# Optimization experiments

Hardware: AMD Instinct MI355X
Metric: run time of the kernel (lower is better)

Reference implementation:

```python
import jax, jax.numpy as jnp
import numpy as np

S, B, D, H, DFF = 1024, 4, 1024, 16, 4096
HD = D // H
EPS = 1e-5


def setup_inputs() -> dict:
    key = jax.random.key(0)
    ks = jax.random.split(key, 16)

    def w(k, shape):
        return jax.random.normal(k, shape, jnp.float32) * 0.02

    inp = {
        "input": jax.random.normal(ks[0], (S, B, D), jnp.float32),  # [seq, batch, d_model]
        "enc": jax.random.normal(ks[1], (S, B, D), jnp.float32),
    }
    i = 2
    for pfx in ("sa", "ca"):
        for name in ("wq", "wk", "wv", "wo"):
            inp[f"{pfx}_{name}"] = w(ks[i], (D, D)); i += 1
            inp[f"{pfx}_b{name[1]}"] = jnp.zeros((D,), jnp.float32)
    inp["w1"] = w(ks[i], (DFF, D)); i += 1
    inp["b1"] = jnp.zeros((DFF,), jnp.float32)
    inp["w2"] = w(ks[i], (D, DFF)); i += 1
    inp["b2"] = jnp.zeros((D,), jnp.float32)
    for n in (1, 2, 3):
        inp[f"ln{n}_g"] = jnp.ones((D,), jnp.float32)
        inp[f"ln{n}_b"] = jnp.zeros((D,), jnp.float32)
    return inp


def _layernorm(x, g, b):
    m = x.mean(-1, keepdims=True)
    v = x.var(-1, keepdims=True)
    return (x - m) * jax.lax.rsqrt(v + EPS) * g + b


def _mha(query, key, value, wq, bq, wk, bk, wv, bv, wo, bo):
    # query/key/value: [seq, batch, d_model] (seq-first layout)
    def proj(x, w, b):
        y = x @ w.T + b
        s, bsz, _ = y.shape
        return y.reshape(s, bsz, H, HD)  # [s, b, h, hd]

    q = proj(query, wq, bq)
    k = proj(key, wk, bk)
    v = proj(value, wv, bv)
    scores = jnp.einsum("sbhd,tbhd->bhst", q, k) / (HD ** 0.5)  # [b, h, s_q, s_k]
    p = jax.nn.softmax(scores, axis=-1)
    o = jnp.einsum("bhst,tbhd->sbhd", p, v)  # [s_q, b, h, hd]
    o = o.reshape(o.shape[0], o.shape[1], D)  # heads concatenated along features
    return o @ wo.T + bo  # [s_q, b, d_model]


def reference(input, enc,
              sa_wq, sa_bq, sa_wk, sa_bk, sa_wv, sa_bv, sa_wo, sa_bo,
              ca_wq, ca_bq, ca_wk, ca_bk, ca_wv, ca_bv, ca_wo, ca_bo,
              w1, b1, w2, b2,
              ln1_g, ln1_b, ln2_g, ln2_b, ln3_g, ln3_b):
    # self-attention: attn_in_1(input, input, input) -> q=k=v=input
    out1 = _mha(input, input, input, sa_wq, sa_bq, sa_wk, sa_bk, sa_wv, sa_bv, sa_wo, sa_bo)
    out = _layernorm(input + out1, ln1_g, ln1_b)
    # cross-attention: attn_in_2(out, enc, enc) binds key=out, query=enc, value=enc
    out2 = _mha(enc, out, enc, ca_wq, ca_bq, ca_wk, ca_bk, ca_wv, ca_bv, ca_wo, ca_bo)
    out = _layernorm(out + out2, ln2_g, ln2_b)
    # FFN (dropout is identity at p=0 / eval)
    out3 = jax.nn.relu(out @ w1.T + b1) @ w2.T + b2
    return _layernorm(out + out3, ln3_g, ln3_b)
```

## Files before the change

kernel.cpp:

```cpp
#include <hip/hip_runtime.h>
#include <hip/hip_bf16.h>
#include <cstdint>
#include <cstddef>


typedef __bf16 bf16;
typedef __attribute__((ext_vector_type(8))) __bf16 bf16x8;
typedef __attribute__((ext_vector_type(4))) __bf16 bf16x4;
typedef __attribute__((ext_vector_type(4))) float f32x4;

#define SEQ   1024
#define BATCH 4
#define DMOD  1024
#define NHEAD 16
#define HDIM  64
#define NTOK  (SEQ*BATCH)
#define DFF   4096

#define GLD(gp, lp) __builtin_amdgcn_global_load_lds( \
    (__attribute__((address_space(1))) void*)(gp),    \
    (__attribute__((address_space(3))) void*)(lp), 16, 0, 0)

struct CastSeg { const float* src; bf16* dst; int n4; };
struct CastArgs { CastSeg seg[12]; };

__global__ __launch_bounds__(256) void cast_multi(CastArgs a) {
  CastSeg s = a.seg[blockIdx.y];
  int i = blockIdx.x * 256 + threadIdx.x;
  if (i < s.n4) {
    float4 v = ((const float4*)s.src)[i];
    bf16x4 o; o[0] = (bf16)v.x; o[1] = (bf16)v.y; o[2] = (bf16)v.z; o[3] = (bf16)v.w;
    ((bf16x4*)s.dst)[i] = o;
  }
}

__global__ __launch_bounds__(256) void gemm_nt(
    const bf16* __restrict__ A, const bf16* __restrict__ W,
    const float* __restrict__ b0, const float* __restrict__ b1,
    const float* __restrict__ b2, const float* __restrict__ b3,
    void* __restrict__ C, int M, int N, int K, int flags, int kc)
{
  __shared__ bf16 As[4096];
  __shared__ bf16 Bs[4096];
  const int tid  = threadIdx.x;
  const int wave = tid >> 6, lane = tid & 63;
  const int quad = lane >> 4, l16 = lane & 15;
  const int m0 = blockIdx.y * 128, n0 = blockIdx.x * 128;
  const int wm = (wave >> 1) * 64, wn = (wave & 1) * 64;

  f32x4 acc[4][4] = {};

  const int srow = tid >> 2;
  const int scol = ((tid & 3) ^ ((srow >> 1) & 3)) * 8;
  const int kbeg = blockIdx.z * kc;
  const bf16* Ap = A + (size_t)(m0 + srow) * K + scol + kbeg;
  const bf16* Wp = W + (size_t)(n0 + srow) * K + scol + kbeg;
  const size_t rstep = (size_t)64 * K;
  bf16* AsW = As + wave * 512;
  bf16* BsW = Bs + wave * 512;

  const int swz = (l16 >> 1) & 3;
  const int aq = (quad ^ swz) * 8;

  for (int k0 = 0; k0 < kc; k0 += 32) {
    __syncthreads();
    GLD(Ap + k0,         AsW);
    GLD(Ap + rstep + k0, AsW + 2048);
    GLD(Wp + k0,         BsW);
    GLD(Wp + rstep + k0, BsW + 2048);
    __syncthreads();
    bf16x8 af[4], bfr[4];
#pragma unroll
    for (int i = 0; i < 4; ++i)
      af[i] = *(const bf16x8*)(As + (wm + i * 16 + l16) * 32 + aq);
#pragma unroll
    for (int i = 0; i < 4; ++i)
      bfr[i] = *(const bf16x8*)(Bs + (wn + i * 16 + l16) * 32 + aq);
#pragma unroll
    for (int mi = 0; mi < 4; ++mi)
#pragma unroll
      for (int ni = 0; ni < 4; ++ni)
        acc[mi][ni] = __builtin_amdgcn_mfma_f32_16x16x32_bf16(af[mi], bfr[ni], acc[mi][ni], 0, 0, 0);
  }

  if (gridDim.z > 1) {
    float* Cp = (float*)C + (size_t)blockIdx.z * M * N;
#pragma unroll
    for (int mi = 0; mi < 4; ++mi) {
      const int gr = m0 + wm + mi * 16 + quad * 4;
#pragma unroll
      for (int ni = 0; ni < 4; ++ni) {
        const int gc = n0 + wn + ni * 16 + l16;
#pragma unroll
        for (int r = 0; r < 4; ++r)
          Cp[(size_t)(gr + r) * N + gc] = acc[mi][ni][r];
      }
    }
    return;
  }

  const float* bp[4] = {b0, b1, b2, b3};
  const bool obf = flags & 1, orelu = flags & 2, oscale = flags & 4;
#pragma unroll
  for (int mi = 0; mi < 4; ++mi) {
    const int gr = m0 + wm + mi * 16 + quad * 4;
#pragma unroll
    for (int ni = 0; ni < 4; ++ni) {
      const int gc = n0 + wn + ni * 16 + l16;
      const float bi = bp[gc >> 10][gc & 1023];
      const float sc = (oscale && gc < 1024) ? 0.125f : 1.0f;
#pragma unroll
      for (int r = 0; r < 4; ++r) {
        float v = (acc[mi][ni][r] + bi) * sc;
        if (orelu) v = fmaxf(v, 0.0f);
        const size_t idx = (size_t)(gr + r) * N + gc;
        if (obf) ((bf16*)C)[idx] = (bf16)v;
        else     ((float*)C)[idx] = v;
      }
    }
  }
}

__global__ __launch_bounds__(256) void vtrans(
    const bf16* __restrict__ V, int ldv, bf16* __restrict__ VT)
{
  const int tid = threadIdx.x, w = tid >> 6, lane = tid & 63;
  const int b = blockIdx.y >> 4;
  const int co = (blockIdx.y & 15) * HDIM;
  const int s0 = blockIdx.x * 64;
  const int hd0 = blockIdx.z * 32 + w * 8;
  bf16x8 v = *(const bf16x8*)(V + ((size_t)(s0 + lane) * BATCH + b) * ldv + co + hd0);
  const size_t obase = ((size_t)blockIdx.y * HDIM + hd0) * SEQ + s0 + lane;
#pragma unroll
  for (int j = 0; j < 8; ++j)
    VT[obase + (size_t)j * SEQ] = v[j];
}

__global__ __launch_bounds__(256) void attn_kernel(
    const bf16* __restrict__ Q, int ldq,
    const bf16* __restrict__ K, int ldk,
    const bf16* __restrict__ VT,
    bf16* __restrict__ O)
{
  __shared__ bf16 Kt[64 * 64];
  __shared__ bf16 Vt[64 * 64];

  const int tid = threadIdx.x, w = tid >> 6, lane = tid & 63;
  const int quad = lane >> 4, l16 = lane & 15;
  const int bh = blockIdx.y, b = bh >> 4;
  const int co = (bh & 15) * HDIM;
  const int sq0 = blockIdx.x * 128 + w * 32;

  bf16x8 qf[2][2];
#pragma unroll
  for (int u = 0; u < 2; ++u) {
    const bf16* qp = Q + ((size_t)(sq0 + u * 16 + l16) * BATCH + b) * ldq + co + quad * 8;
    qf[u][0] = *(const bf16x8*)qp;
    qf[u][1] = *(const bf16x8*)(qp + 32);
  }

  f32x4 oacc[2][4] = {};
  float lsum[2] = {0.f, 0.f};

  const int srow = lane >> 3;
  const int glog = (lane & 7) ^ srow;
  const int sw = l16 & 7;

  for (int t0 = 0; t0 < SEQ; t0 += 64) {
    __syncthreads();
#pragma unroll
    for (int j = 0; j < 2; ++j) {
      const int slot = j * 32 + w * 8 + srow;
      const int m = slot & 15, half = (slot >> 4) & 1, chunk = slot >> 5;
      const int t = chunk * 32 + 8 * (m >> 2) + 4 * half + (m & 3);
      GLD(K + ((size_t)(t0 + t) * BATCH + b) * ldk + co + glog * 8,
          Kt + (j * 32 + w * 8) * 64);
      const int hd = j * 32 + w * 8 + srow;
      GLD(VT + ((size_t)bh * HDIM + hd) * SEQ + t0 + glog * 8,
          Vt + (j * 32 + w * 8) * 64);
    }
    __syncthreads();

#pragma unroll
    for (int c = 0; c < 2; ++c) {
      const bf16* k0 = Kt + (c * 32 + l16) * 64;
      const bf16* k1 = Kt + (c * 32 + 16 + l16) * 64;
      const int g0 = (quad ^ sw) * 8;
      const int g1 = ((4 + quad) ^ sw) * 8;
      bf16x8 ka00 = *(const bf16x8*)(k0 + g0);
      bf16x8 ka01 = *(const bf16x8*)(k0 + g1);
      bf16x8 ka10 = *(const bf16x8*)(k1 + g0);
      bf16x8 ka11 = *(const bf16x8*)(k1 + g1);
      bf16x8 vf[4];
#pragma unroll
      for (int nt = 0; nt < 4; ++nt)
        vf[nt] = *(const bf16x8*)(Vt + (nt * 16 + l16) * 64 + (((c * 4 + quad) ^ sw) * 8));
#pragma unroll
      for (int u = 0; u < 2; ++u) {
        f32x4 c0 = {}, c1 = {};
        c0 = __builtin_amdgcn_mfma_f32_16x16x32_bf16(ka00, qf[u][0], c0, 0, 0, 0);
        c0 = __builtin_amdgcn_mfma_f32_16x16x32_bf16(ka01, qf[u][1], c0, 0, 0, 0);
        c1 = __builtin_amdgcn_mfma_f32_16x16x32_bf16(ka10, qf[u][0], c1, 0, 0, 0);
        c1 = __builtin_amdgcn_mfma_f32_16x16x32_bf16(ka11, qf[u][1], c1, 0, 0, 0);
        bf16x8 pf; float ls = 0.f;
#pragma unroll
        for (int r = 0; r < 4; ++r) {
          float p0 = __expf(c0[r]);
          float p1 = __expf(c1[r]);
          ls += p0 + p1;
          pf[r] = (bf16)p0;
          pf[4 + r] = (bf16)p1;
        }
        lsum[u] += ls;
#pragma unroll
        for (int nt = 0; nt < 4; ++nt)
          oacc[u][nt] = __builtin_amdgcn_mfma_f32_16x16x32_bf16(pf, vf[nt], oacc[u][nt], 0, 0, 0);
      }
    }
  }

#pragma unroll
  for (int u = 0; u < 2; ++u) {
    float s = lsum[u];
    s += __shfl_xor(s, 16, 64);
    s += __shfl_xor(s, 32, 64);
#pragma unroll
    for (int r = 0; r < 4; ++r) {
      const float inv = 1.0f / __shfl(s, quad * 4 + r, 64);
      const size_t ro = ((size_t)(sq0 + u * 16 + quad * 4 + r) * BATCH + b) * DMOD + co;
#pragma unroll
      for (int nt = 0; nt < 4; ++nt)
        O[ro + nt * 16 + l16] = (bf16)(oacc[u][nt][r] * inv);
    }
  }
}

__global__ __launch_bounds__(256) void add_ln_red(
    const float* __restrict__ Xa,
    const float* __restrict__ p0, const float* __restrict__ p1,
    const float* __restrict__ p2, const float* __restrict__ p3, int np,
    const float* __restrict__ bias,
    const float* __restrict__ g, const float* __restrict__ beta,
    float* __restrict__ outf, bf16* __restrict__ outb)
{
  const int row = blockIdx.x, tid = threadIdx.x;
  const size_t base = (size_t)row * DMOD;
  float4 a = ((const float4*)(Xa + base))[tid];
  float4 q0 = ((const float4*)(p0 + base))[tid];
  float4 q1 = ((const float4*)(p1 + base))[tid];
  float x0 = a.x + q0.x + q1.x, x1 = a.y + q0.y + q1.y;
  float x2 = a.z + q0.z + q1.z, x3 = a.w + q0.w + q1.w;
  if (np > 2) {
    float4 q2 = ((const float4*)(p2 + base))[tid];
    float4 q3 = ((const float4*)(p3 + base))[tid];
    x0 += q2.x + q3.x; x1 += q2.y + q3.y; x2 += q2.z + q3.z; x3 += q2.w + q3.w;
  }
  float4 bi = ((const float4*)bias)[tid];
  x0 += bi.x; x1 += bi.y; x2 += bi.z; x3 += bi.w;

  float s  = x0 + x1 + x2 + x3;
  float s2 = x0 * x0 + x1 * x1 + x2 * x2 + x3 * x3;
#pragma unroll
  for (int m = 1; m < 64; m <<= 1) { s += __shfl_xor(s, m, 64); s2 += __shfl_xor(s2, m, 64); }
  __shared__ float red[8];
  if ((tid & 63) == 0) { red[tid >> 6] = s; red[4 + (tid >> 6)] = s2; }
  __syncthreads();
  s  = red[0] + red[1] + red[2] + red[3];
  s2 = red[4] + red[5] + red[6] + red[7];
  const float mean = s * (1.0f / DMOD);
  const float var  = s2 * (1.0f / DMOD) - mean * mean;
  const float rs   = rsqrtf(var + 1e-5f);
  float4 gv = ((const float4*)g)[tid];
  float4 bv = ((const float4*)beta)[tid];
  float y0 = (x0 - mean) * rs * gv.x + bv.x;
  float y1 = (x1 - mean) * rs * gv.y + bv.y;
  float y2 = (x2 - mean) * rs * gv.z + bv.z;
  float y3 = (x3 - mean) * rs * gv.w + bv.w;
  float4 o; o.x = y0; o.y = y1; o.z = y2; o.w = y3;
  ((float4*)(outf + base))[tid] = o;
  if (outb) {
    bf16x4 ob; ob[0] = (bf16)y0; ob[1] = (bf16)y1; ob[2] = (bf16)y2; ob[3] = (bf16)y3;
    ((bf16x4*)(outb + base))[tid] = ob;
  }
}

__global__ __launch_bounds__(256) void reduce_cast(
    const float* __restrict__ p0, const float* __restrict__ p1,
    const float* __restrict__ bias, bf16* __restrict__ out)
{
  const int row = blockIdx.x, tid = threadIdx.x;
  const size_t base = (size_t)row * DMOD;
  float4 a = ((const float4*)(p0 + base))[tid];
  float4 b = ((const float4*)(p1 + base))[tid];
  float4 bi = ((const float4*)bias)[tid];
  bf16x4 o;
  o[0] = (bf16)(a.x + b.x + bi.x); o[1] = (bf16)(a.y + b.y + bi.y);
  o[2] = (bf16)(a.z + b.z + bi.z); o[3] = (bf16)(a.w + b.w + bi.w);
  ((bf16x4*)(out + base))[tid] = o;
}

extern "C" void kernel_launch(void* const* d_in, const int* in_sizes, int n_in,
                              void* d_out, int out_size, void* d_ws, size_t ws_size,
                              hipStream_t stream)
{
  const float* x0    = (const float*)d_in[0];
  const float* enc   = (const float*)d_in[1];
  const float* sa_wq = (const float*)d_in[2];
  const float* sa_bq = (const float*)d_in[3];
  const float* sa_wk = (const float*)d_in[4];
  const float* sa_bk = (const float*)d_in[5];
  const float* sa_wv = (const float*)d_in[6];
  const float* sa_bv = (const float*)d_in[7];
  const float* sa_wo = (const float*)d_in[8];
  const float* sa_bo = (const float*)d_in[9];
  const float* ca_wq = (const float*)d_in[10];
  const float* ca_bq = (const float*)d_in[11];
  const float* ca_wk = (const float*)d_in[12];
  const float* ca_bk = (const float*)d_in[13];
  const float* ca_wv = (const float*)d_in[14];
  const float* ca_bv = (const float*)d_in[15];
  const float* ca_wo = (const float*)d_in[16];
  const float* ca_bo = (const float*)d_in[17];
  const float* w1    = (const float*)d_in[18];
  const float* b1    = (const float*)d_in[19];
  const float* w2    = (const float*)d_in[20];
  const float* b2    = (const float*)d_in[21];
  const float* ln1g  = (const float*)d_in[22];
  const float* ln1b  = (const float*)d_in[23];
  const float* ln2g  = (const float*)d_in[24];
  const float* ln2b  = (const float*)d_in[25];
  const float* ln3g  = (const float*)d_in[26];
  const float* ln3b  = (const float*)d_in[27];

  char* ws = (char*)d_ws;
  size_t off = 0;
  auto take = [&](size_t bytes) -> char* {
    char* p = ws + off; off += (bytes + 255) & ~(size_t)255; return p;
  };
  const size_t WEL = (size_t)DMOD * DMOD;
  const size_t ACT = (size_t)NTOK * DMOD;
  bf16*  Wqkv_s = (bf16*)take(3 * WEL * 2);
  bf16*  Wo_s   = (bf16*)take(WEL * 2);
  bf16*  Wqv_c  = (bf16*)take(2 * WEL * 2);
  bf16*  Wk_c   = (bf16*)take(WEL * 2);
  bf16*  Wo_c   = (bf16*)take(WEL * 2);
  bf16*  W1b    = (bf16*)take(4 * WEL * 2);
  bf16*  W2b    = (bf16*)take(4 * WEL * 2);
  char*  regP   = take(32 * 1024 * 1024);
  bf16*  x0b    = (bf16*)regP;
  bf16*  QKVs   = (bf16*)(regP + 8 * 1024 * 1024);
  float* part0  = (float*)regP;
  float* part1  = (float*)(regP + 16 * 1024 * 1024);
  bf16*  QVc    = (bf16*)regP;
  bf16*  Kc     = (bf16*)(regP + 16 * 1024 * 1024);
  char*  regE   = take(16 * 1024 * 1024);
  bf16*  encb   = (bf16*)regE;
  bf16*  ctx    = (bf16*)(regE + 8 * 1024 * 1024);
  float* part3  = (float*)regE;
  float* out1f  = (float*)take(ACT * 4);
  float* part2  = out1f;
  bf16*  out1b  = (bf16*)take(ACT * 2);
  float* out2f  = (float*)take(ACT * 4);
  bf16*  out2b  = (bf16*)take(ACT * 2);
  char*  regH   = take((size_t)NTOK * DFF * 2);
  bf16*  Hff    = (bf16*)regH;
  float* wkp0   = (float*)regH;
  float* wkp1   = (float*)(regH + 16 * 1024 * 1024);
  bf16*  VT     = (bf16*)take(ACT * 2);
  (void)ws_size; (void)in_sizes; (void)n_in; (void)out_size;

  CastArgs cargs;
  const int nw  = (int)(WEL / 4);
  const int ntk = (int)(ACT / 4);
  cargs.seg[0]  = {x0,    x0b,            ntk};
  cargs.seg[1]  = {enc,   encb,           ntk};
  cargs.seg[2]  = {sa_wq, Wqkv_s,         nw};
  cargs.seg[3]  = {sa_wk, Wqkv_s + WEL,   nw};
  cargs.seg[4]  = {sa_wv, Wqkv_s + 2*WEL, nw};
  cargs.seg[5]  = {sa_wo, Wo_s,           nw};
  cargs.seg[6]  = {ca_wq, Wqv_c,          nw};
  cargs.seg[7]  = {ca_wv, Wqv_c + WEL,    nw};
  cargs.seg[8]  = {ca_wk, Wk_c,           nw};
  cargs.seg[9]  = {ca_wo, Wo_c,           nw};
  cargs.seg[10] = {w1,    W1b,            nw * 4};
  cargs.seg[11] = {w2,    W2b,            nw * 4};
  cast_multi<<<dim3((ntk + 255) / 256, 12), 256, 0, stream>>>(cargs);

  auto gemm = [&](const bf16* A, const bf16* Wt,
                  const float* bb0, const float* bb1, const float* bb2, const float* bb3,
                  void* Cp, int M, int N, int Kd, int flags, int nz) {
    gemm_nt<<<dim3(N / 128, M / 128, nz), 256, 0, stream>>>(
        A, Wt, bb0, bb1, bb2, bb3, Cp, M, N, Kd, flags, Kd / nz);
  };

  gemm(x0b, Wqkv_s, sa_bq, sa_bk, sa_bv, sa_bv, QKVs, NTOK, 3 * DMOD, DMOD, 1 | 4, 1);
  vtrans<<<dim3(SEQ / 64, BATCH * NHEAD, 2), 256, 0, stream>>>(QKVs + 2 * DMOD, 3 * DMOD, VT);
  attn_kernel<<<dim3(SEQ / 128, BATCH * NHEAD), 256, 0, stream>>>(
      QKVs, 3 * DMOD, QKVs + DMOD, 3 * DMOD, VT, ctx);
  gemm(ctx, Wo_s, nullptr, nullptr, nullptr, nullptr, part0, NTOK, DMOD, DMOD, 0, 2);
  add_ln_red<<<dim3(NTOK), 256, 0, stream>>>(x0, part0, part1, nullptr, nullptr, 2,
                                             sa_bo, ln1g, ln1b, out1f, out1b);
  gemm(encb, Wqv_c, ca_bq, ca_bv, ca_bv, ca_bv, QVc, NTOK, 2 * DMOD, DMOD, 1 | 4, 1);
  gemm(out1b, Wk_c, nullptr, nullptr, nullptr, nullptr, wkp0, NTOK, DMOD, DMOD, 0, 2);
  reduce_cast<<<dim3(NTOK), 256, 0, stream>>>(wkp0, wkp1, ca_bk, Kc);
  vtrans<<<dim3(SEQ / 64, BATCH * NHEAD, 2), 256, 0, stream>>>(QVc + DMOD, 2 * DMOD, VT);
  attn_kernel<<<dim3(SEQ / 128, BATCH * NHEAD), 256, 0, stream>>>(
      QVc, 2 * DMOD, Kc, DMOD, VT, ctx);
  gemm(ctx, Wo_c, nullptr, nullptr, nullptr, nullptr, part0, NTOK, DMOD, DMOD, 0, 2);
  add_ln_red<<<dim3(NTOK), 256, 0, stream>>>(out1f, part0, part1, nullptr, nullptr, 2,
                                             ca_bo, ln2g, ln2b, out2f, out2b);
  gemm(out2b, W1b, b1, b1 + 1024, b1 + 2048, b1 + 3072, Hff, NTOK, DFF, DMOD, 1 | 2, 1);
  gemm(Hff, W2b, nullptr, nullptr, nullptr, nullptr, part0, NTOK, DMOD, DFF, 0, 4);
  add_ln_red<<<dim3(NTOK), 256, 0, stream>>>(out2f, part0, part1, part2, part3, 4,
                                             b2, ln3g, ln3b, (float*)d_out, nullptr);
}
```

Measured before the change: 563.1 us.

## Swap MFMA operands for vector epilogue stores and remap blocks for XCD locality

The GEMM now feeds the weight tile as the A operand of the MFMA, so each lane's four accumulator values are consecutive output columns. The epilogue can then write them with 16-byte float4 or 8-byte bf16x4 stores and read the bias as one float4, instead of issuing scalar strided stores. Separately, the linear block index is remapped so each of the 8 residue classes (lin & 7) gets a contiguous band of M tiles. The likely aim is to keep A-row reuse within one XCD's L2. The remap assumes gridDim.y is divisible by 8.

```diff
diff --git a/kernel.cpp b/kernel.cpp
--- a/kernel.cpp
+++ b/kernel.cpp
@@ -45,14 +45,23 @@
   const int tid  = threadIdx.x;
   const int wave = tid >> 6, lane = tid & 63;
   const int quad = lane >> 4, l16 = lane & 15;
-  const int m0 = blockIdx.y * 128, n0 = blockIdx.x * 128;
+
+  const int nbx = gridDim.x, nby = gridDim.y, nbz = gridDim.z;
+  const int lin = blockIdx.x + nbx * (blockIdx.y + nby * blockIdx.z);
+  const int c = lin & 7;
+  int q = lin >> 3;
+  const int bx = q % nbx; q /= nbx;
+  const int bz = q % nbz; q /= nbz;
+  const int by = c * (nby >> 3) + q;
+
+  const int m0 = by * 128, n0 = bx * 128;
   const int wm = (wave >> 1) * 64, wn = (wave & 1) * 64;
 
   f32x4 acc[4][4] = {};
 
   const int srow = tid >> 2;
   const int scol = ((tid & 3) ^ ((srow >> 1) & 3)) * 8;
-  const int kbeg = blockIdx.z * kc;
+  const int kbeg = bz * kc;
   const bf16* Ap = A + (size_t)(m0 + srow) * K + scol + kbeg;
   const bf16* Wp = W + (size_t)(n0 + srow) * K + scol + kbeg;
   const size_t rstep = (size_t)64 * K;
@@ -69,31 +78,29 @@
     GLD(Wp + k0,         BsW);
     GLD(Wp + rstep + k0, BsW + 2048);
     __syncthreads();
-    bf16x8 af[4], bfr[4];
+    bf16x8 wf[4], tf[4];
 #pragma unroll
     for (int i = 0; i < 4; ++i)
-      af[i] = *(const bf16x8*)(As + (wm + i * 16 + l16) * 32 + aq);
+      wf[i] = *(const bf16x8*)(Bs + (wn + i * 16 + l16) * 32 + aq);
 #pragma unroll
     for (int i = 0; i < 4; ++i)
-      bfr[i] = *(const bf16x8*)(Bs + (wn + i * 16 + l16) * 32 + aq);
+      tf[i] = *(const bf16x8*)(As + (wm + i * 16 + l16) * 32 + aq);
 #pragma unroll
     for (int mi = 0; mi < 4; ++mi)
 #pragma unroll
       for (int ni = 0; ni < 4; ++ni)
-        acc[mi][ni] = __builtin_amdgcn_mfma_f32_16x16x32_bf16(af[mi], bfr[ni], acc[mi][ni], 0, 0, 0);
+        acc[mi][ni] = __builtin_amdgcn_mfma_f32_16x16x32_bf16(wf[mi], tf[ni], acc[mi][ni], 0, 0, 0);
   }
 
   if (gridDim.z > 1) {
-    float* Cp = (float*)C + (size_t)blockIdx.z * M * N;
-#pragma unroll
-    for (int mi = 0; mi < 4; ++mi) {
-      const int gr = m0 + wm + mi * 16 + quad * 4;
-#pragma unroll
-      for (int ni = 0; ni < 4; ++ni) {
-        const int gc = n0 + wn + ni * 16 + l16;
-#pragma unroll
-        for (int r = 0; r < 4; ++r)
-          Cp[(size_t)(gr + r) * N + gc] = acc[mi][ni][r];
+    float* Cp = (float*)C + (size_t)bz * M * N;
+#pragma unroll
+    for (int ni = 0; ni < 4; ++ni) {
+      const size_t rowb = (size_t)(m0 + wm + ni * 16 + l16) * N;
+#pragma unroll
+      for (int mi = 0; mi < 4; ++mi) {
+        const int gf = n0 + wn + mi * 16 + quad * 4;
+        *(f32x4*)(Cp + rowb + gf) = acc[mi][ni];
       }
     }
     return;
@@ -102,20 +109,27 @@
   const float* bp[4] = {b0, b1, b2, b3};
   const bool obf = flags & 1, orelu = flags & 2, oscale = flags & 4;
 #pragma unroll
-  for (int mi = 0; mi < 4; ++mi) {
-    const int gr = m0 + wm + mi * 16 + quad * 4;
-#pragma unroll
-    for (int ni = 0; ni < 4; ++ni) {
-      const int gc = n0 + wn + ni * 16 + l16;
-      const float bi = bp[gc >> 10][gc & 1023];
-      const float sc = (oscale && gc < 1024) ? 0.125f : 1.0f;
-#pragma unroll
-      for (int r = 0; r < 4; ++r) {
-        float v = (acc[mi][ni][r] + bi) * sc;
-        if (orelu) v = fmaxf(v, 0.0f);
-        const size_t idx = (size_t)(gr + r) * N + gc;
-        if (obf) ((bf16*)C)[idx] = (bf16)v;
-        else     ((float*)C)[idx] = v;
+  for (int ni = 0; ni < 4; ++ni) {
+    const size_t rowb = (size_t)(m0 + wm + ni * 16 + l16) * N;
+#pragma unroll
+    for (int mi = 0; mi < 4; ++mi) {
+      const int gf = n0 + wn + mi * 16 + quad * 4;
+      const float4 bi = *(const float4*)(bp[gf >> 10] + (gf & 1023));
+      const float sc = (oscale && gf < 1024) ? 0.125f : 1.0f;
+      float v0 = (acc[mi][ni][0] + bi.x) * sc;
+      float v1 = (acc[mi][ni][1] + bi.y) * sc;
+      float v2 = (acc[mi][ni][2] + bi.z) * sc;
+      float v3 = (acc[mi][ni][3] + bi.w) * sc;
+      if (orelu) {
+        v0 = fmaxf(v0, 0.f); v1 = fmaxf(v1, 0.f);
+        v2 = fmaxf(v2, 0.f); v3 = fmaxf(v3, 0.f);
+      }
+      if (obf) {
+        bf16x4 o; o[0] = (bf16)v0; o[1] = (bf16)v1; o[2] = (bf16)v2; o[3] = (bf16)v3;
+        *(bf16x4*)((bf16*)C + rowb + gf) = o;
+      } else {
+        float4 o; o.x = v0; o.y = v1; o.z = v2; o.w = v3;
+        *(float4*)((float*)C + rowb + gf) = o;
       }
     }
   }
```

After: 559.0 us. About the same (-0.7%).
